# Optimization experiments

Measured on AMD Instinct MI355X. Metric: run time of the kernel, lower is better.

Reference implementation:

```python
import jax, jax.numpy as jnp
import numpy as np

BN_EPS = 1e-5


def conv1x1(x, W, b):
    # x: [B, Cin, N], W: [Cout, Cin], b: [Cout]
    return jnp.einsum('oc,bcn->bon', W, x) + b[None, :, None]


def bn(x, p):
    # p: [4, C] rows = gamma, beta, running_mean, running_var (inference BN)
    g, be, m, v = p[0], p[1], p[2], p[3]
    inv = jax.lax.rsqrt(v + BN_EPS)
    return (x - m[None, :, None]) * (g * inv)[None, :, None] + be[None, :, None]


def conv_bn_relu(x, W, b, p):
    return jax.nn.relu(bn(conv1x1(x, W, b), p))


def _make_params(key, cout, cin):
    k1, k2 = jax.random.split(key)
    W = jax.random.normal(k1, (cout, cin), jnp.float32) * (1.0 / np.sqrt(cin))
    b = jax.random.normal(k2, (cout,), jnp.float32) * 0.01
    p = jnp.stack([jnp.ones(cout), jnp.zeros(cout), jnp.zeros(cout), jnp.ones(cout)]).astype(jnp.float32)
    return W, b, p


def setup_inputs() -> dict:
    key = jax.random.key(0)
    ks = jax.random.split(key, 16)
    B, N, S, D1, D2 = 2, 16384, 4096, 128, 256
    Cin, C, Cm = D1 + D2 + 13, 128, 128  # 397, out_channel, mlp[0]
    inp = {
        'xyz1': jax.random.normal(ks[0], (B, N, 3), jnp.float32),
        'xyz2': jax.random.normal(ks[1], (B, S, 3), jnp.float32),
        'points1': jax.random.normal(ks[2], (B, D1, N), jnp.float32),
        'points2': jax.random.normal(ks[3], (B, D2, S), jnp.float32),
        'last_pred': jax.random.normal(ks[4], (B, S, 13), jnp.float32),
    }
    inp['fuse_W'], inp['fuse_b'], inp['fuse_bn'] = _make_params(ks[5], C, Cin)
    inp['ext1_W'], inp['ext1_b'], inp['ext1_bn'] = _make_params(ks[6], C, C)
    inp['ext2_W'], inp['ext2_b'], inp['ext2_bn'] = _make_params(ks[7], C, C)
    inp['pred1_W'], inp['pred1_b'], inp['pred1_bn'] = _make_params(ks[8], Cm, C)
    inp['pred2_W'], inp['pred2_b'], inp['pred2_bn'] = _make_params(ks[9], 13, Cm)
    return inp


def _forward(xyz1, xyz2, points1, points2, last_pred,
             fuse_W, fuse_b, fuse_bn, ext1_W, ext1_b, ext1_bn,
             ext2_W, ext2_b, ext2_bn, pred1_W, pred1_b, pred1_bn,
             pred2_W, pred2_b, pred2_bn):
    B, N, _ = xyz1.shape
    p1 = jnp.transpose(points1, (0, 2, 1))  # [B, N, D1]
    p2 = jnp.transpose(points2, (0, 2, 1))  # [B, S, D2]
    # squared distances [B, N, S]
    dists = (jnp.sum(xyz1 ** 2, -1)[:, :, None]
             + jnp.sum(xyz2 ** 2, -1)[:, None, :]
             - 2.0 * jnp.einsum('bnc,bsc->bns', xyz1, xyz2))
    # 3 smallest distances (partial top-k instead of full sort; same math)
    neg_d3, idx = jax.lax.top_k(-dists, 3)  # [B, N, 3]
    d3 = -neg_d3
    recip = 1.0 / (d3 + 1e-8)
    weight = recip / jnp.sum(recip, axis=2, keepdims=True)  # [B, N, 3]
    bidx = jnp.arange(B)[:, None, None]
    interp_pts = jnp.sum(p2[bidx, idx] * weight[..., None], axis=2)        # [B, N, D2]
    interp_pred = jnp.sum(last_pred[bidx, idx] * weight[..., None], axis=2)  # [B, N, 13]
    new_points = jnp.transpose(jnp.concatenate([p1, interp_pts, interp_pred], axis=-1), (0, 2, 1))  # [B, Cin, N]
    # fuse
    x = conv_bn_relu(new_points, fuse_W, fuse_b, fuse_bn)
    # extraction: one ConvBNReLURes1D block (groups=1, res_expansion=1)
    h = conv_bn_relu(x, ext1_W, ext1_b, ext1_bn)
    x = jax.nn.relu(bn(conv1x1(h, ext2_W, ext2_b), ext2_bn) + x)  # [B, C, N]
    new_points_out = x
    # prediction head (dropout is identity in eval mode)
    feat = conv_bn_relu(x, pred1_W, pred1_b, pred1_bn)
    pred = conv_bn_relu(feat, pred2_W, pred2_b, pred2_bn)
    return (new_points_out,
            jnp.transpose(feat, (0, 2, 1)),
            jnp.transpose(pred, (0, 2, 1)))


def reference(xyz1, xyz2, points1, points2, last_pred,
              fuse_W, fuse_b, fuse_bn, ext1_W, ext1_b, ext1_bn,
              ext2_W, ext2_b, ext2_bn, pred1_W, pred1_b, pred1_bn,
              pred2_W, pred2_b, pred2_bn):
    return _forward(xyz1, xyz2, points1, points2, last_pred,
                    fuse_W, fuse_b, fuse_bn, ext1_W, ext1_b, ext1_bn,
                    ext2_W, ext2_b, ext2_bn, pred1_W, pred1_b, pred1_bn,
                    pred2_W, pred2_b, pred2_bn)
```

## Files before the change

kernel.cpp:

```cpp
#include <hip/hip_runtime.h>
#include <stdint.h>

#define B_   2
#define N_   16384
#define S_   4096
#define D2_  256
#define CIN_ 397
#define KP_  416
#define C_   128
#define OC_  13
#define NCHUNK_ 16
#define CHS_ (S_ / NCHUNK_)
#define NCAND_ (NCHUNK_ * 3)
#define XQ_P 272

typedef unsigned short u16;
typedef unsigned int u32;
typedef short s16x8 __attribute__((ext_vector_type(8)));
typedef float f32x4 __attribute__((ext_vector_type(4)));
typedef float f32x2 __attribute__((ext_vector_type(2)));

#define MFMA16(a, b, c) __builtin_amdgcn_mfma_f32_16x16x32_bf16((a), (b), (c), 0, 0, 0)

__device__ __forceinline__ float b2f(u16 h) {
  union { unsigned int u; float f; } v; v.u = ((unsigned int)h) << 16; return v.f;
}
__device__ __forceinline__ u16 f2b(float f) {
  union { float f; unsigned int u; } v; v.f = f;
  unsigned int r = v.u + 0x7fffu + ((v.u >> 16) & 1u);
  return (u16)(r >> 16);
}

#define INS3M(k0, k1, k2, key)                                            \
  do {                                                                    \
    u32 _m1, _m2;                                                         \
    asm("v_med3_u32 %0, %1, %2, %3" : "=v"(_m1) : "v"(k0), "v"(k1), "v"(key)); \
    asm("v_med3_u32 %0, %1, %2, %3" : "=v"(_m2) : "v"(k1), "v"(k2), "v"(key)); \
    k0 = min(k0, key);                                                    \
    k1 = _m1;                                                             \
    k2 = _m2;                                                             \
  } while (0)

__device__ __forceinline__ void transpose_body(
    const float* __restrict__ in, u16* __restrict__ out,
    int C, int S, int opitch, int b, int s0, int c0,
    float* __restrict__ tile, int tr, int tc4) {
  const float* ip = in + (size_t)b * C * S;
  u16* op = out + (size_t)b * S * opitch;
#pragma unroll
  for (int r = 0; r < 64; r += 16) {
    float4 v = *(const float4*)(ip + (size_t)(c0 + tr + r) * S + s0 + tc4);
    tile[(tr + r) * 65 + tc4 + 0] = v.x;
    tile[(tr + r) * 65 + tc4 + 1] = v.y;
    tile[(tr + r) * 65 + tc4 + 2] = v.z;
    tile[(tr + r) * 65 + tc4 + 3] = v.w;
  }
  __syncthreads();
#pragma unroll
  for (int r = 0; r < 64; r += 16) {
    ushort4 v;
    v.x = f2b(tile[(tc4 + 0) * 65 + tr + r]);
    v.y = f2b(tile[(tc4 + 1) * 65 + tr + r]);
    v.z = f2b(tile[(tc4 + 2) * 65 + tr + r]);
    v.w = f2b(tile[(tc4 + 3) * 65 + tr + r]);
    *(ushort4*)(op + (size_t)(s0 + tr + r) * opitch + c0 + tc4) = v;
  }
}

__global__ __launch_bounds__(256) void setup_scan_kernel(
    const float* __restrict__ xyz1, const float* __restrict__ xyz2,
    const float* __restrict__ points2,
    const float* __restrict__ fW, const float* __restrict__ fb,
    const float* __restrict__ fbn,
    const float* __restrict__ e1W, const float* __restrict__ e1b,
    const float* __restrict__ e1bn,
    const float* __restrict__ e2W, const float* __restrict__ e2b,
    const float* __restrict__ e2bn,
    const float* __restrict__ p1W, const float* __restrict__ p1b,
    const float* __restrict__ p1bn,
    const float* __restrict__ p2W, const float* __restrict__ p2b,
    const float* __restrict__ p2bn,
    u16* __restrict__ cand, u16* __restrict__ p2t,
    u16* __restrict__ Wf, u16* __restrict__ W1o,
    u16* __restrict__ W2o, u16* __restrict__ W3o,
    u16* __restrict__ Wp2, float* __restrict__ st) {
  __shared__ __align__(16) float smem[64 * 65];
  int id = blockIdx.x;
  int tid = threadIdx.x;

  if (id < 512) {
    float* xs = smem;
    float* ys = smem + 256;
    float* zs = smem + 512;
    float* nw = smem + 768;
    int chunk = id & 15;
    int ny = (id >> 4) & 15;
    int b = id >> 8;
    int s0 = chunk * CHS_;
    const float* x2 = xyz2 + ((size_t)b * S_ + s0) * 3;
    {
      float xx = x2[tid * 3], yy = x2[tid * 3 + 1], zz = x2[tid * 3 + 2];
      xs[tid] = xx; ys[tid] = yy; zs[tid] = zz;
      nw[tid] = -0.5f * fmaf(xx, xx, fmaf(yy, yy, zz * zz));
    }
    __syncthreads();
    int nA = ny * 1024 + tid;
    float qx[4], qy[4], qz[4], n1[4];
#pragma unroll
    for (int q = 0; q < 4; ++q) {
      const float* x1 = xyz1 + ((size_t)b * N_ + nA + q * 256) * 3;
      qx[q] = x1[0]; qy[q] = x1[1]; qz[q] = x1[2];
      n1[q] = fmaf(qx[q], qx[q], fmaf(qy[q], qy[q], qz[q] * qz[q]));
    }
    u32 K[4][2][3];
#pragma unroll
    for (int q = 0; q < 4; ++q)
#pragma unroll
      for (int e = 0; e < 2; ++e)
#pragma unroll
        for (int r = 0; r < 3; ++r) K[q][e][r] = ~0u;
    f32x2 m2 = {-2.f, -2.f}, z2 = {0.f, 0.f};
#pragma unroll 2
    for (int s = 0; s < CHS_; s += 2) {
      f32x2 px = *(const f32x2*)(xs + s);
      f32x2 py = *(const f32x2*)(ys + s);
      f32x2 pz = *(const f32x2*)(zs + s);
      f32x2 pw = *(const f32x2*)(nw + s);
#pragma unroll
      for (int q = 0; q < 4; ++q) {
        f32x2 ax2 = {qx[q], qx[q]}, ay2 = {qy[q], qy[q]}, az2 = {qz[q], qz[q]};
        f32x2 n12 = {n1[q], n1[q]};
        f32x2 d = __builtin_elementwise_fma(az2, pz, pw);
        d = __builtin_elementwise_fma(ay2, py, d);
        d = __builtin_elementwise_fma(ax2, px, d);
        d = __builtin_elementwise_fma(m2, d, n12);
        d = __builtin_elementwise_max(d, z2);
        u32 k0 = (__float_as_uint(d[0]) & 0xFFFFFF00u) | (u32)s;
        u32 k1 = (__float_as_uint(d[1]) & 0xFFFFFF00u) | (u32)(s + 1);
        INS3M(K[q][0][0], K[q][0][1], K[q][0][2], k0);
        INS3M(K[q][1][0], K[q][1][1], K[q][1][2], k1);
      }
    }
#pragma unroll
    for (int q = 0; q < 4; ++q) {
      INS3M(K[q][0][0], K[q][0][1], K[q][0][2], K[q][1][0]);
      INS3M(K[q][0][0], K[q][0][1], K[q][0][2], K[q][1][1]);
      INS3M(K[q][0][0], K[q][0][1], K[q][0][2], K[q][1][2]);
      u16* co = cand + ((size_t)(b * N_ + nA + q * 256)) * NCAND_ + chunk * 3;
      co[0] = (u16)((K[q][0][0] & 0xFFu) + s0);
      co[1] = (u16)((K[q][0][1] & 0xFFu) + s0);
      co[2] = (u16)((K[q][0][2] & 0xFFu) + s0);
    }
    return;
  }

  int tr = tid >> 4;
  int tc4 = (tid & 15) * 4;
  if (id < 1024) {
    int id2 = id - 512;
    int sx = id2 & 63, sy = (id2 >> 6) & 3, b = id2 >> 8;
    transpose_body(points2, p2t, 256, S_, 256, b, sx * 64, sy * 64, smem, tr, tc4);
    return;
  }
  int t = (id - 1024) * 256 + tid;
  int stride = 64 * 256;
  for (int i = t; i < 128 * KP_; i += stride) {
    int m = i / KP_, k = i - m * KP_;
    Wf[i] = (k < CIN_) ? f2b(fW[m * CIN_ + k]) : (u16)0;
  }
  for (int i = t; i < 128 * 128; i += stride) {
    W1o[i] = f2b(e1W[i]);
    W2o[i] = f2b(e2W[i]);
    W3o[i] = f2b(p1W[i]);
  }
  for (int i = t; i < 16 * 128; i += stride) {
    int m = i >> 7;
    Wp2[i] = (m < OC_) ? f2b(p2W[i]) : (u16)0;
  }
  for (int i = t; i < 5 * 128; i += stride) {
    int sg = i >> 7, c = i & 127;
    const float* bn; const float* bc; int Cc = 128;
    switch (sg) {
      case 0: bn = fbn;  bc = fb;  break;
      case 1: bn = e1bn; bc = e1b; break;
      case 2: bn = e2bn; bc = e2b; break;
      case 3: bn = p1bn; bc = p1b; break;
      default: bn = p2bn; bc = p2b; Cc = OC_; break;
    }
    float s = 0.f, tt = 0.f;
    if (c < Cc) {
      float g  = bn[0 * Cc + c], be = bn[1 * Cc + c];
      float mu = bn[2 * Cc + c], vv = bn[3 * Cc + c];
      float inv = 1.0f / sqrtf(vv + 1e-5f);
      s = g * inv;
      tt = (bc[c] - mu) * s + be;
    }
    st[sg * 256 + c] = s;
    st[sg * 256 + 128 + c] = tt;
  }
}

__device__ __forceinline__ void ins3(double d, int i,
                                     double& D0, double& D1, double& D2,
                                     int& I0, int& I1, int& I2) {
  if ((d < D2) || (d == D2 && i < I2)) {
    if ((d < D1) || (d == D1 && i < I1)) {
      D2 = D1; I2 = I1;
      if ((d < D0) || (d == D0 && i < I0)) { D1 = D0; I1 = I0; D0 = d; I0 = i; }
      else                                  { D1 = d; I1 = i; }
    } else { D2 = d; I2 = i; }
  }
}

__global__ __launch_bounds__(256) void interp_kernel(
    const float* __restrict__ xyz1, const float* __restrict__ xyz2,
    const u16* __restrict__ cand, const u16* __restrict__ p2t,
    const float* __restrict__ last_pred, u16* __restrict__ xq) {
  __shared__ int   iS[32][3];
  __shared__ float wS[32][3];
  int id = blockIdx.x;
  int b = id >> 9;
  int n0 = (id & 511) * 32;
  int tid = threadIdx.x;

  {
#pragma clang fp contract(off)
    int qi = tid >> 3, part = tid & 7;
    int qg = b * N_ + n0 + qi;
    const u16* ci = cand + (size_t)qg * NCAND_ + part * 6;
    const float* x2b = xyz2 + (size_t)b * S_ * 3;
    int ii[6];
#pragma unroll
    for (int j = 0; j < 6; ++j) ii[j] = ci[j];
    float pcx[6], pcy[6], pcz[6];
#pragma unroll
    for (int j = 0; j < 6; ++j) {
      const float* p = x2b + (size_t)ii[j] * 3;
      pcx[j] = p[0]; pcy[j] = p[1]; pcz[j] = p[2];
    }
    const float* x1 = xyz1 + (size_t)qg * 3;
    double ax = x1[0], ay = x1[1], az = x1[2];
    double n1 = (ax * ax + ay * ay) + az * az;
    double D0 = 1e300, D1 = 1e300, D2v = 1e300;
    int I0 = 2147483647, I1 = 2147483647, I2 = 2147483647;
#pragma unroll
    for (int j = 0; j < 6; ++j) {
      double px = pcx[j], py = pcy[j], pz = pcz[j];
      double n2 = (px * px + py * py) + pz * pz;
      double dot = (ax * px + ay * py) + az * pz;
      double d = (n1 + n2) - 2.0 * dot;
      ins3(d, ii[j], D0, D1, D2v, I0, I1, I2);
    }
#pragma unroll
    for (int r = 0; r < 3; ++r) {
      int m = 1 << r;
      double e0 = __shfl_xor(D0, m);
      double e1 = __shfl_xor(D1, m);
      double e2 = __shfl_xor(D2v, m);
      int j0 = __shfl_xor(I0, m);
      int j1 = __shfl_xor(I1, m);
      int j2 = __shfl_xor(I2, m);
      ins3(e0, j0, D0, D1, D2v, I0, I1, I2);
      ins3(e1, j1, D0, D1, D2v, I0, I1, I2);
      ins3(e2, j2, D0, D1, D2v, I0, I1, I2);
    }
    if (part == 0) {
      double r0 = 1.0 / (D0 + 1e-8);
      double r1 = 1.0 / (D1 + 1e-8);
      double r2 = 1.0 / (D2v + 1e-8);
      double sum = (r0 + r1) + r2;
      wS[qi][0] = (float)(r0 / sum);
      wS[qi][1] = (float)(r1 / sum);
      wS[qi][2] = (float)(r2 / sum);
      iS[qi][0] = I0; iS[qi][1] = I1; iS[qi][2] = I2;
    }
  }
  __syncthreads();

  int wv = tid >> 6, lane = tid & 63;
  int q = wv * 8 + (lane >> 3);
  int cg = lane & 7;
  int n = n0 + q;
  int i0 = iS[q][0], i1 = iS[q][1], i2 = iS[q][2];
  float w0 = wS[q][0], w1 = wS[q][1], w2 = wS[q][2];
  const u16* p2b = p2t + (size_t)b * S_ * D2_;
  const u16* r0p = p2b + (size_t)i0 * D2_ + cg * 32;
  const u16* r1p = p2b + (size_t)i1 * D2_ + cg * 32;
  const u16* r2p = p2b + (size_t)i2 * D2_ + cg * 32;
  u16* xrow = xq + (size_t)(b * N_ + n) * XQ_P;
#pragma unroll
  for (int j = 0; j < 8; ++j) {
    ushort4 a = *(const ushort4*)(r0p + j * 4);
    ushort4 e = *(const ushort4*)(r1p + j * 4);
    ushort4 c = *(const ushort4*)(r2p + j * 4);
    ushort4 v;
    v.x = f2b((w0 * b2f(a.x) + w1 * b2f(e.x)) + w2 * b2f(c.x));
    v.y = f2b((w0 * b2f(a.y) + w1 * b2f(e.y)) + w2 * b2f(c.y));
    v.z = f2b((w0 * b2f(a.z) + w1 * b2f(e.z)) + w2 * b2f(c.z));
    v.w = f2b((w0 * b2f(a.w) + w1 * b2f(e.w)) + w2 * b2f(c.w));
    *(ushort4*)(xrow + cg * 32 + j * 4) = v;
  }
  if (cg == 0) {
    const float* lpb = last_pred + (size_t)b * S_ * OC_;
    u16 pv[16];
#pragma unroll
    for (int c = 0; c < 16; ++c) pv[c] = 0;
#pragma unroll
    for (int c = 0; c < OC_; ++c) {
      float l0 = lpb[(size_t)i0 * OC_ + c];
      float l1 = lpb[(size_t)i1 * OC_ + c];
      float l2 = lpb[(size_t)i2 * OC_ + c];
      pv[c] = f2b((w0 * l0 + w1 * l1) + w2 * l2);
    }
#pragma unroll
    for (int c4 = 0; c4 < 4; ++c4) {
      *(ushort4*)(xrow + 256 + c4 * 4) =
          make_ushort4(pv[c4 * 4], pv[c4 * 4 + 1], pv[c4 * 4 + 2], pv[c4 * 4 + 3]);
    }
  }
}

__device__ __forceinline__ void gemm32(const u16* __restrict__ W, const u16* xb,
                                       int l15, int lq, int wv, f32x4 acc[2][2]) {
#pragma unroll
  for (int mtl = 0; mtl < 2; ++mtl) {
    acc[mtl][0] = (f32x4){0.f, 0.f, 0.f, 0.f};
    acc[mtl][1] = (f32x4){0.f, 0.f, 0.f, 0.f};
  }
#pragma unroll
  for (int ks = 0; ks < 4; ++ks) {
    int ko = ks * 32 + lq * 8;
    s16x8 b0 = *(const s16x8*)(xb + l15 * 136 + ko);
    s16x8 b1 = *(const s16x8*)(xb + (16 + l15) * 136 + ko);
#pragma unroll
    for (int mtl = 0; mtl < 2; ++mtl) {
      s16x8 a = *(const s16x8*)(W + (size_t)((wv * 2 + mtl) * 16 + l15) * 128 + ko);
      acc[mtl][0] = MFMA16(a, b0, acc[mtl][0]);
      acc[mtl][1] = MFMA16(a, b1, acc[mtl][1]);
    }
  }
}

__global__ __launch_bounds__(256, 4) void gemm_kernel(
    const float* __restrict__ points1, const u16* __restrict__ xq,
    const u16* __restrict__ Wf,
    const u16* __restrict__ W1, const u16* __restrict__ W2,
    const u16* __restrict__ W3, const u16* __restrict__ Wp2,
    const float* __restrict__ st, float* __restrict__ out) {
  __shared__ __align__(16) u16 xb0[32 * 136];
  __shared__ __align__(16) u16 xb1[32 * 136];
  int b = blockIdx.y;
  int n0 = blockIdx.x * 32;
  int tid = threadIdx.x;
  int wv = tid >> 6, lane = tid & 63;
  int l15 = lane & 15, lq = lane >> 4;
  f32x4 acc[2][2];

  {
    int n4 = (tid & 7) * 4;
    int cb = tid >> 3;
    const float* p1b = points1 + (size_t)b * C_ * N_;
#pragma unroll
    for (int rep = 0; rep < 4; ++rep) {
      int c = cb + rep * 32;
      float4 v = *(const float4*)(p1b + (size_t)c * N_ + n0 + n4);
      xb1[(n4 + 0) * 136 + c] = f2b(v.x);
      xb1[(n4 + 1) * 136 + c] = f2b(v.y);
      xb1[(n4 + 2) * 136 + c] = f2b(v.z);
      xb1[(n4 + 3) * 136 + c] = f2b(v.w);
    }
  }
  __syncthreads();

#pragma unroll
  for (int mtl = 0; mtl < 2; ++mtl) {
    acc[mtl][0] = (f32x4){0.f, 0.f, 0.f, 0.f};
    acc[mtl][1] = (f32x4){0.f, 0.f, 0.f, 0.f};
  }
  {
#pragma unroll 2
    for (int ks = 0; ks < 4; ++ks) {
      int ko = ks * 32 + lq * 8;
      s16x8 bf0 = *(const s16x8*)(&xb1[l15 * 136 + ko]);
      s16x8 bf1 = *(const s16x8*)(&xb1[(16 + l15) * 136 + ko]);
#pragma unroll
      for (int mtl = 0; mtl < 2; ++mtl) {
        s16x8 a = *(const s16x8*)(Wf + (size_t)((wv * 2 + mtl) * 16 + l15) * KP_ + ko);
        acc[mtl][0] = MFMA16(a, bf0, acc[mtl][0]);
        acc[mtl][1] = MFMA16(a, bf1, acc[mtl][1]);
      }
    }
    const u16* qrow0 = xq + ((size_t)(b * N_ + n0 + l15)) * XQ_P;
    const u16* qrow1 = qrow0 + (size_t)16 * XQ_P;
#pragma unroll 3
    for (int ks = 0; ks < 9; ++ks) {
      int col = ks * 32 + lq * 8;
      s16x8 bf0 = {0, 0, 0, 0, 0, 0, 0, 0};
      s16x8 bf1 = {0, 0, 0, 0, 0, 0, 0, 0};
      if (ks < 8 || lq < 2) {
        bf0 = *(const s16x8*)(qrow0 + col);
        bf1 = *(const s16x8*)(qrow1 + col);
      }
#pragma unroll
      for (int mtl = 0; mtl < 2; ++mtl) {
        s16x8 a = *(const s16x8*)(Wf + (size_t)((wv * 2 + mtl) * 16 + l15) * KP_ + 128 + col);
        acc[mtl][0] = MFMA16(a, bf0, acc[mtl][0]);
        acc[mtl][1] = MFMA16(a, bf1, acc[mtl][1]);
      }
    }
  }
  __syncthreads();
#pragma unroll
  for (int mtl = 0; mtl < 2; ++mtl) {
    int m4 = (wv * 2 + mtl) * 16 + lq * 4;
    f32x4 sc = *(const f32x4*)(st + 0 * 256 + m4);
    f32x4 bi = *(const f32x4*)(st + 0 * 256 + 128 + m4);
#pragma unroll
    for (int nt = 0; nt < 2; ++nt) {
      int n_l = nt * 16 + l15;
      ushort4 v;
      v.x = f2b(fmaxf(acc[mtl][nt][0] * sc[0] + bi[0], 0.f));
      v.y = f2b(fmaxf(acc[mtl][nt][1] * sc[1] + bi[1], 0.f));
      v.z = f2b(fmaxf(acc[mtl][nt][2] * sc[2] + bi[2], 0.f));
      v.w = f2b(fmaxf(acc[mtl][nt][3] * sc[3] + bi[3], 0.f));
      *(ushort4*)(&xb0[n_l * 136 + m4]) = v;
    }
  }
  __syncthreads();

  gemm32(W1, xb0, l15, lq, wv, acc);
#pragma unroll
  for (int mtl = 0; mtl < 2; ++mtl) {
    int m4 = (wv * 2 + mtl) * 16 + lq * 4;
    f32x4 sc = *(const f32x4*)(st + 1 * 256 + m4);
    f32x4 bi = *(const f32x4*)(st + 1 * 256 + 128 + m4);
#pragma unroll
    for (int nt = 0; nt < 2; ++nt) {
      int n_l = nt * 16 + l15;
      ushort4 v;
      v.x = f2b(fmaxf(acc[mtl][nt][0] * sc[0] + bi[0], 0.f));
      v.y = f2b(fmaxf(acc[mtl][nt][1] * sc[1] + bi[1], 0.f));
      v.z = f2b(fmaxf(acc[mtl][nt][2] * sc[2] + bi[2], 0.f));
      v.w = f2b(fmaxf(acc[mtl][nt][3] * sc[3] + bi[3], 0.f));
      *(ushort4*)(&xb1[n_l * 136 + m4]) = v;
    }
  }
  __syncthreads();

  gemm32(W2, xb1, l15, lq, wv, acc);
#pragma unroll
  for (int mtl = 0; mtl < 2; ++mtl) {
    int m4 = (wv * 2 + mtl) * 16 + lq * 4;
    f32x4 sc = *(const f32x4*)(st + 2 * 256 + m4);
    f32x4 bi = *(const f32x4*)(st + 2 * 256 + 128 + m4);
#pragma unroll
    for (int nt = 0; nt < 2; ++nt) {
      int n_l = nt * 16 + l15;
      int n_g = n0 + n_l;
      ushort4 xp = *(const ushort4*)(&xb0[n_l * 136 + m4]);
      float v0 = fmaxf(acc[mtl][nt][0] * sc[0] + bi[0] + b2f(xp.x), 0.f);
      float v1 = fmaxf(acc[mtl][nt][1] * sc[1] + bi[1] + b2f(xp.y), 0.f);
      float v2 = fmaxf(acc[mtl][nt][2] * sc[2] + bi[2] + b2f(xp.z), 0.f);
      float v3 = fmaxf(acc[mtl][nt][3] * sc[3] + bi[3] + b2f(xp.w), 0.f);
      ushort4 v;
      v.x = f2b(v0); v.y = f2b(v1); v.z = f2b(v2); v.w = f2b(v3);
      *(ushort4*)(&xb0[n_l * 136 + m4]) = v;
      out[((size_t)(b * C_ + m4 + 0)) * N_ + n_g] = v0;
      out[((size_t)(b * C_ + m4 + 1)) * N_ + n_g] = v1;
      out[((size_t)(b * C_ + m4 + 2)) * N_ + n_g] = v2;
      out[((size_t)(b * C_ + m4 + 3)) * N_ + n_g] = v3;
    }
  }
  __syncthreads();

  gemm32(W3, xb0, l15, lq, wv, acc);
  {
    float* out1 = out + (size_t)B_ * C_ * N_;
#pragma unroll
    for (int mtl = 0; mtl < 2; ++mtl) {
      int m4 = (wv * 2 + mtl) * 16 + lq * 4;
      f32x4 sc = *(const f32x4*)(st + 3 * 256 + m4);
      f32x4 bi = *(const f32x4*)(st + 3 * 256 + 128 + m4);
#pragma unroll
      for (int nt = 0; nt < 2; ++nt) {
        int n_l = nt * 16 + l15;
        int n_g = n0 + n_l;
        float v0 = fmaxf(acc[mtl][nt][0] * sc[0] + bi[0], 0.f);
        float v1 = fmaxf(acc[mtl][nt][1] * sc[1] + bi[1], 0.f);
        float v2 = fmaxf(acc[mtl][nt][2] * sc[2] + bi[2], 0.f);
        float v3 = fmaxf(acc[mtl][nt][3] * sc[3] + bi[3], 0.f);
        ushort4 v;
        v.x = f2b(v0); v.y = f2b(v1); v.z = f2b(v2); v.w = f2b(v3);
        *(ushort4*)(&xb1[n_l * 136 + m4]) = v;
        float4 o4 = make_float4(v0, v1, v2, v3);
        *(float4*)(out1 + ((size_t)(b * N_ + n_g)) * 128 + m4) = o4;
      }
    }
  }
  __syncthreads();

  if (wv < 2) {
    f32x4 a2 = (f32x4){0.f, 0.f, 0.f, 0.f};
#pragma unroll
    for (int ks = 0; ks < 4; ++ks) {
      int ko = ks * 32 + lq * 8;
      s16x8 b0 = *(const s16x8*)(&xb1[(wv * 16 + l15) * 136 + ko]);
      s16x8 a = *(const s16x8*)(Wp2 + (size_t)l15 * 128 + ko);
      a2 = MFMA16(a, b0, a2);
    }
    float* out2 = out + (size_t)B_ * C_ * N_ + (size_t)B_ * N_ * 128;
    f32x4 sc = *(const f32x4*)(st + 4 * 256 + lq * 4);
    f32x4 bi = *(const f32x4*)(st + 4 * 256 + 128 + lq * 4);
    int n_g = n0 + wv * 16 + l15;
#pragma unroll
    for (int r = 0; r < 4; ++r) {
      int m = lq * 4 + r;
      if (m < OC_) {
        out2[((size_t)(b * N_ + n_g)) * OC_ + m] =
            fmaxf(a2[r] * sc[r] + bi[r], 0.f);
      }
    }
  }
}

extern "C" void kernel_launch(void* const* d_in, const int* in_sizes, int n_in,
                              void* d_out, int out_size, void* d_ws, size_t ws_size,
                              hipStream_t stream) {
  const float* xyz1      = (const float*)d_in[0];
  const float* xyz2      = (const float*)d_in[1];
  const float* points1   = (const float*)d_in[2];
  const float* points2   = (const float*)d_in[3];
  const float* last_pred = (const float*)d_in[4];
  const float* fuse_W    = (const float*)d_in[5];
  const float* fuse_b    = (const float*)d_in[6];
  const float* fuse_bn   = (const float*)d_in[7];
  const float* ext1_W    = (const float*)d_in[8];
  const float* ext1_b    = (const float*)d_in[9];
  const float* ext1_bn   = (const float*)d_in[10];
  const float* ext2_W    = (const float*)d_in[11];
  const float* ext2_b    = (const float*)d_in[12];
  const float* ext2_bn   = (const float*)d_in[13];
  const float* pred1_W   = (const float*)d_in[14];
  const float* pred1_b   = (const float*)d_in[15];
  const float* pred1_bn  = (const float*)d_in[16];
  const float* pred2_W   = (const float*)d_in[17];
  const float* pred2_b   = (const float*)d_in[18];
  const float* pred2_bn  = (const float*)d_in[19];

  char* ws = (char*)d_ws;
  u16*   p2t  = (u16*)(ws + 0);
  u16*   cand = (u16*)(ws + 4194304);
  u16*   Wf   = (u16*)(ws + 7340032);
  u16*   W1   = (u16*)(ws + 7446528);
  u16*   W2   = (u16*)(ws + 7479296);
  u16*   W3   = (u16*)(ws + 7512064);
  u16*   Wp2  = (u16*)(ws + 7544832);
  float* st   = (float*)(ws + 7548928);
  u16*   xq   = (u16*)(ws + 7554048);

  setup_scan_kernel<<<dim3(1088), dim3(256), 0, stream>>>(
      xyz1, xyz2, points2,
      fuse_W, fuse_b, fuse_bn, ext1_W, ext1_b, ext1_bn, ext2_W, ext2_b, ext2_bn,
      pred1_W, pred1_b, pred1_bn, pred2_W, pred2_b, pred2_bn,
      cand, p2t, Wf, W1, W2, W3, Wp2, st);

  interp_kernel<<<dim3(1024), dim3(256), 0, stream>>>(
      xyz1, xyz2, cand, p2t, last_pred, xq);

  gemm_kernel<<<dim3(N_ / 32, B_), dim3(256), 0, stream>>>(
      points1, xq, Wf, W1, W2, W3, Wp2, st, (float*)d_out);
}
```

Measured before the change: 221.1 us.

## Software-pipeline KNN scan LDS loads and store candidates chunk-major as ushort4

The brute-force nearest-neighbour scan now loads 8 reference points at a time with 128-bit LDS reads, double-buffering two register sets so the next batch is fetched while the current one is processed. The shared-memory arrays are padded to 272 floats to shift their bank alignment. Candidate indices are written in a chunk-major layout, padded to 4 per entry and stored as one ushort4, so both the stores and the interpolation kernel's reads become coalesced vector accesses. The price is more workspace and more live registers in the scan loop, which can lower occupancy.

```diff
diff --git a/kernel.cpp b/kernel.cpp
--- a/kernel.cpp
+++ b/kernel.cpp
@@ -11,7 +11,6 @@
 #define OC_  13
 #define NCHUNK_ 16
 #define CHS_ (S_ / NCHUNK_)
-#define NCAND_ (NCHUNK_ * 3)
 #define XQ_P 272
 
 typedef unsigned short u16;
@@ -40,6 +39,9 @@
     k1 = _m1;                                                             \
     k2 = _m2;                                                             \
   } while (0)
+
+#define SHL(v) __builtin_shufflevector((v), (v), 0, 1)
+#define SHH(v) __builtin_shufflevector((v), (v), 2, 3)
 
 __device__ __forceinline__ void transpose_body(
     const float* __restrict__ in, u16* __restrict__ out,
@@ -90,9 +92,9 @@
 
   if (id < 512) {
     float* xs = smem;
-    float* ys = smem + 256;
-    float* zs = smem + 512;
-    float* nw = smem + 768;
+    float* ys = smem + 272;
+    float* zs = smem + 544;
+    float* nw = smem + 816;
     int chunk = id & 15;
     int ny = (id >> 4) & 15;
     int b = id >> 8;
@@ -120,36 +122,61 @@
 #pragma unroll
         for (int r = 0; r < 3; ++r) K[q][e][r] = ~0u;
     f32x2 m2 = {-2.f, -2.f}, z2 = {0.f, 0.f};
-#pragma unroll 2
-    for (int s = 0; s < CHS_; s += 2) {
-      f32x2 px = *(const f32x2*)(xs + s);
-      f32x2 py = *(const f32x2*)(ys + s);
-      f32x2 pz = *(const f32x2*)(zs + s);
-      f32x2 pw = *(const f32x2*)(nw + s);
-#pragma unroll
-      for (int q = 0; q < 4; ++q) {
-        f32x2 ax2 = {qx[q], qx[q]}, ay2 = {qy[q], qy[q]}, az2 = {qz[q], qz[q]};
-        f32x2 n12 = {n1[q], n1[q]};
-        f32x2 d = __builtin_elementwise_fma(az2, pz, pw);
-        d = __builtin_elementwise_fma(ay2, py, d);
-        d = __builtin_elementwise_fma(ax2, px, d);
-        d = __builtin_elementwise_fma(m2, d, n12);
-        d = __builtin_elementwise_max(d, z2);
-        u32 k0 = (__float_as_uint(d[0]) & 0xFFFFFF00u) | (u32)s;
-        u32 k1 = (__float_as_uint(d[1]) & 0xFFFFFF00u) | (u32)(s + 1);
-        INS3M(K[q][0][0], K[q][0][1], K[q][0][2], k0);
-        INS3M(K[q][1][0], K[q][1][1], K[q][1][2], k1);
-      }
-    }
+
+#define LOAD8(X0, X1, Y0, Y1, Z0, Z1, W0, W1, sb)                         \
+    do {                                                                  \
+      X0 = *(const f32x4*)(xs + (sb));  X1 = *(const f32x4*)(xs + (sb) + 4); \
+      Y0 = *(const f32x4*)(ys + (sb));  Y1 = *(const f32x4*)(ys + (sb) + 4); \
+      Z0 = *(const f32x4*)(zs + (sb));  Z1 = *(const f32x4*)(zs + (sb) + 4); \
+      W0 = *(const f32x4*)(nw + (sb));  W1 = *(const f32x4*)(nw + (sb) + 4); \
+    } while (0)
+
+#define PAIR_Q(PX, PY, PZ, PW, sidx)                                      \
+    do {                                                                  \
+      _Pragma("unroll")                                                   \
+      for (int q = 0; q < 4; ++q) {                                       \
+        f32x2 ax2 = {qx[q], qx[q]}, ay2 = {qy[q], qy[q]};                 \
+        f32x2 az2 = {qz[q], qz[q]}, n12 = {n1[q], n1[q]};                 \
+        f32x2 d = __builtin_elementwise_fma(az2, PZ, PW);                 \
+        d = __builtin_elementwise_fma(ay2, PY, d);                        \
+        d = __builtin_elementwise_fma(ax2, PX, d);                        \
+        d = __builtin_elementwise_fma(m2, d, n12);                        \
+        d = __builtin_elementwise_max(d, z2);                             \
+        u32 k0 = (__float_as_uint(d[0]) & 0xFFFFFF00u) | (u32)(sidx);     \
+        u32 k1 = (__float_as_uint(d[1]) & 0xFFFFFF00u) | (u32)((sidx) + 1); \
+        INS3M(K[q][0][0], K[q][0][1], K[q][0][2], k0);                    \
+        INS3M(K[q][1][0], K[q][1][1], K[q][1][2], k1);                    \
+      }                                                                   \
+    } while (0)
+
+#define COMPUTE8(X0, X1, Y0, Y1, Z0, Z1, W0, W1, base)                    \
+    do {                                                                  \
+      PAIR_Q(SHL(X0), SHL(Y0), SHL(Z0), SHL(W0), (base));                 \
+      PAIR_Q(SHH(X0), SHH(Y0), SHH(Z0), SHH(W0), (base) + 2);             \
+      PAIR_Q(SHL(X1), SHL(Y1), SHL(Z1), SHL(W1), (base) + 4);             \
+      PAIR_Q(SHH(X1), SHH(Y1), SHH(Z1), SHH(W1), (base) + 6);             \
+    } while (0)
+
+    f32x4 AX0, AX1, AY0, AY1, AZ0, AZ1, AW0, AW1;
+    f32x4 BX0, BX1, BY0, BY1, BZ0, BZ1, BW0, BW1;
+    LOAD8(AX0, AX1, AY0, AY1, AZ0, AZ1, AW0, AW1, 0);
+#pragma unroll 1
+    for (int s8 = 0; s8 < CHS_; s8 += 16) {
+      LOAD8(BX0, BX1, BY0, BY1, BZ0, BZ1, BW0, BW1, s8 + 8);
+      COMPUTE8(AX0, AX1, AY0, AY1, AZ0, AZ1, AW0, AW1, s8);
+      LOAD8(AX0, AX1, AY0, AY1, AZ0, AZ1, AW0, AW1, s8 + 16);
+      COMPUTE8(BX0, BX1, BY0, BY1, BZ0, BZ1, BW0, BW1, s8 + 8);
+    }
+
 #pragma unroll
     for (int q = 0; q < 4; ++q) {
       INS3M(K[q][0][0], K[q][0][1], K[q][0][2], K[q][1][0]);
       INS3M(K[q][0][0], K[q][0][1], K[q][0][2], K[q][1][1]);
       INS3M(K[q][0][0], K[q][0][1], K[q][0][2], K[q][1][2]);
-      u16* co = cand + ((size_t)(b * N_ + nA + q * 256)) * NCAND_ + chunk * 3;
-      co[0] = (u16)((K[q][0][0] & 0xFFu) + s0);
-      co[1] = (u16)((K[q][0][1] & 0xFFu) + s0);
-      co[2] = (u16)((K[q][0][2] & 0xFFu) + s0);
+      u16* co = cand + ((size_t)(b * NCHUNK_ + chunk) * N_ + (nA + q * 256)) * 4;
+      *(ushort4*)co = make_ushort4((u16)((K[q][0][0] & 0xFFu) + s0),
+                                   (u16)((K[q][0][1] & 0xFFu) + s0),
+                                   (u16)((K[q][0][2] & 0xFFu) + s0), 0);
     }
     return;
   }
@@ -226,12 +253,14 @@
   {
 #pragma clang fp contract(off)
     int qi = tid >> 3, part = tid & 7;
-    int qg = b * N_ + n0 + qi;
-    const u16* ci = cand + (size_t)qg * NCAND_ + part * 6;
+    int nq = n0 + qi;
+    int qg = b * N_ + nq;
+    ushort4 ca = *(const ushort4*)(cand +
+        ((size_t)(b * NCHUNK_ + 2 * part) * N_ + nq) * 4);
+    ushort4 cbv = *(const ushort4*)(cand +
+        ((size_t)(b * NCHUNK_ + 2 * part + 1) * N_ + nq) * 4);
+    int ii[6] = {ca.x, ca.y, ca.z, cbv.x, cbv.y, cbv.z};
     const float* x2b = xyz2 + (size_t)b * S_ * 3;
-    int ii[6];
-#pragma unroll
-    for (int j = 0; j < 6; ++j) ii[j] = ci[j];
     float pcx[6], pcy[6], pcz[6];
 #pragma unroll
     for (int j = 0; j < 6; ++j) {
@@ -550,13 +579,13 @@
   char* ws = (char*)d_ws;
   u16*   p2t  = (u16*)(ws + 0);
   u16*   cand = (u16*)(ws + 4194304);
-  u16*   Wf   = (u16*)(ws + 7340032);
-  u16*   W1   = (u16*)(ws + 7446528);
-  u16*   W2   = (u16*)(ws + 7479296);
-  u16*   W3   = (u16*)(ws + 7512064);
-  u16*   Wp2  = (u16*)(ws + 7544832);
-  float* st   = (float*)(ws + 7548928);
-  u16*   xq   = (u16*)(ws + 7554048);
+  u16*   Wf   = (u16*)(ws + 8388608);
+  u16*   W1   = (u16*)(ws + 8495104);
+  u16*   W2   = (u16*)(ws + 8527872);
+  u16*   W3   = (u16*)(ws + 8560640);
+  u16*   Wp2  = (u16*)(ws + 8593408);
+  float* st   = (float*)(ws + 8597504);
+  u16*   xq   = (u16*)(ws + 8602624);
 
   setup_scan_kernel<<<dim3(1088), dim3(256), 0, stream>>>(
       xyz1, xyz2, points2,
```

After: 218.9 us. About the same (-1.0%).
